# Optimization experiments

Measured on AMD Instinct MI355X. Metric: run time of the kernel, lower is better.

The kernel has to match this reference:

```python
import jax, jax.numpy as jnp
import numpy as np

B, D = 8192, 1024            # batch, inputs_dim
H1, H2, H3 = 2048, 1024, 512 # expert_units
NS, NT = 8, 4                # num_shared_experts, num_tasks_experts
E = NS + 3 * NT              # 20 experts total: [shared 0:8 | SA 8:12 | RA 12:16 | EA 16:20]
TU1, TU2 = 1024, 512         # tower_units
TIN = H3 * 4                 # tower input dim = 2048


def lrelu(x):
    return jnp.where(x >= 0, x, 0.1 * x)


def setup_inputs() -> dict:
    key = jax.random.key(0)
    ks = jax.random.split(key, 24)
    s = 0.02
    return {
        "inputs": jax.random.normal(ks[0], (B, D), jnp.float32),
        # stacked expert MLP params (leading axis = expert index)
        "W1": jax.random.normal(ks[1], (E, D, H1), jnp.float32) * s,
        "b1": jnp.zeros((E, H1), jnp.float32),
        "W2": jax.random.normal(ks[2], (E, H1, H2), jnp.float32) * s,
        "b2": jnp.zeros((E, H2), jnp.float32),
        "W3": jax.random.normal(ks[3], (E, H2, H3), jnp.float32) * s,
        "b3": jnp.zeros((E, H3), jnp.float32),
        # gate linears (single layer + softmax over dim 1)
        "Wg_sh": jax.random.normal(ks[4], (D, NS + 3 * NT), jnp.float32) * s,
        "bg_sh": jnp.zeros((NS + 3 * NT,), jnp.float32),
        "Wg_sa": jax.random.normal(ks[5], (D, NT + NS), jnp.float32) * s,
        "bg_sa": jnp.zeros((NT + NS,), jnp.float32),
        "Wg_ra": jax.random.normal(ks[6], (D, NT + NS), jnp.float32) * s,
        "bg_ra": jnp.zeros((NT + NS,), jnp.float32),
        "Wg_ea": jax.random.normal(ks[7], (D, NT + NS), jnp.float32) * s,
        "bg_ea": jnp.zeros((NT + NS,), jnp.float32),
        # 2 towers (one per task), stacked on leading axis
        "Wt1": jax.random.normal(ks[8], (2, TIN, TU1), jnp.float32) * s,
        "bt1": jnp.zeros((2, TU1), jnp.float32),
        "Wt2": jax.random.normal(ks[9], (2, TU1, TU2), jnp.float32) * s,
        "bt2": jnp.zeros((2, TU2), jnp.float32),
        # per-task output denses: PRESENCE=6, AIRFLOW=4
        "Wd0": jax.random.normal(ks[10], (TU2, 6), jnp.float32) * s,
        "bd0": jnp.zeros((6,), jnp.float32),
        "Wd1": jax.random.normal(ks[11], (TU2, 4), jnp.float32) * s,
        "bd1": jnp.zeros((4,), jnp.float32),
    }


def reference(inputs, W1, b1, W2, b2, W3, b3,
              Wg_sh, bg_sh, Wg_sa, bg_sa, Wg_ra, bg_ra, Wg_ea, bg_ea,
              Wt1, bt1, Wt2, bt2, Wd0, bd0, Wd1, bd1):
    x = inputs
    # all 20 experts as batched GEMMs: [E, B, h]
    h = lrelu(jnp.einsum('bd,edh->ebh', x, W1) + b1[:, None, :])
    h = lrelu(jnp.einsum('ebh,ehk->ebk', h, W2) + b2[:, None, :])
    eo = lrelu(jnp.einsum('ebk,eko->ebo', h, W3) + b3[:, None, :])  # [E,B,H3]

    # gates (softmax over feature dim)
    g_sh = jax.nn.softmax(x @ Wg_sh + bg_sh, axis=1)  # [B, 20]
    g_sa = jax.nn.softmax(x @ Wg_sa + bg_sa, axis=1)  # [B, 12]
    g_ra = jax.nn.softmax(x @ Wg_ra + bg_ra, axis=1)
    g_ea = jax.nn.softmax(x @ Wg_ea + bg_ea, axis=1)

    # shared gate: order = shared + SA + RA + EA == natural stacking order
    out_sh = jnp.einsum('ebh,be->bh', eo, g_sh)
    # task gates: order = task experts + shared experts
    out_sa = jnp.einsum('ebh,be->bh', jnp.concatenate([eo[NS:NS+NT], eo[:NS]], 0), g_sa)
    out_ra = jnp.einsum('ebh,be->bh', jnp.concatenate([eo[NS+NT:NS+2*NT], eo[:NS]], 0), g_ra)
    out_ea = jnp.einsum('ebh,be->bh', jnp.concatenate([eo[NS+2*NT:], eo[:NS]], 0), g_ea)

    tower_in = jnp.concatenate([out_sh, out_sa, out_ra, out_ea], axis=1)  # [B, 2048]
    t = lrelu(jnp.einsum('bi,kio->kbo', tower_in, Wt1) + bt1[:, None, :])  # [2,B,TU1]
    t = lrelu(jnp.einsum('kbo,kop->kbp', t, Wt2) + bt2[:, None, :])        # [2,B,TU2]
    out0 = t[0] @ Wd0 + bd0  # [B, 6]  PRESENCE
    out1 = t[1] @ Wd1 + bd1  # [B, 4]  AIRFLOW
    return (out0, out1)
```

## Files before the change

kernel.cpp:

```cpp
#include <hip/hip_runtime.h>

#define DEV __device__ __forceinline__

typedef __bf16 bf16x8 __attribute__((ext_vector_type(8)));
typedef float f32x4 __attribute__((ext_vector_type(4)));

DEV unsigned short f2bf(float f) {
  union { float f; unsigned u; } v; v.f = f;
  unsigned r = v.u + 0x7FFFu + ((v.u >> 16) & 1u);
  return (unsigned short)(r >> 16);
}
DEV float bf2f(unsigned short h) {
  union { float f; unsigned u; } v; v.u = ((unsigned)h) << 16;
  return v.f;
}

DEV void gload16(const void* g, void* l) {
  __builtin_amdgcn_global_load_lds(
      (__attribute__((address_space(1))) void*)(g),
      (__attribute__((address_space(3))) void*)(l), 16, 0, 0);
}

__global__ __launch_bounds__(512) void gemm256(
    const unsigned short* __restrict__ A,
    const unsigned short* __restrict__ Bt,
    const float* __restrict__ bias,
    unsigned short* __restrict__ Out,
    int N, int K, int nbx, int nby,
    long sA, long sB, long sBias, long sOut)
{
  int wg = blockIdx.x;
  {
    const int nwg = gridDim.x;
    const int q = nwg >> 3, r = nwg & 7;
    const int xcd = wg & 7, pos = wg >> 3;
    wg = (xcd < r ? xcd * (q + 1) : r * (q + 1) + (xcd - r) * q) + pos;
  }
  const int per_z = nbx * nby;
  const int z  = wg / per_z;
  const int rz = wg - z * per_z;
  const int by = rz / nbx;
  const int bx = rz - by * nbx;

  A    += (size_t)z * sA;
  Bt   += (size_t)z * sB;
  bias += (size_t)z * sBias;
  Out  += (size_t)z * sOut;

  const int tid  = threadIdx.x;
  const int lane = tid & 63;
  const int wid  = tid >> 6;
  const int wm   = wid >> 2, wn = wid & 3;
  const int m0   = by * 256, n0 = bx * 256;

  __shared__ alignas(16) char sm[2][65536];

  f32x4 acc[8][4];
  const f32x4 fz = {0.f, 0.f, 0.f, 0.f};
#pragma unroll
  for (int i = 0; i < 8; ++i)
#pragma unroll
    for (int j = 0; j < 4; ++j) acc[i][j] = fz;

  const size_t ldab = (size_t)K * 2;
  const int rr = tid >> 3;
  const int ch = (tid & 7) ^ (rr & 7);
  const char* gA = (const char*)A  + (size_t)(m0 + rr) * ldab + ch * 16;
  const char* gB = (const char*)Bt + (size_t)(n0 + rr) * ldab + ch * 16;
  const size_t rowStep = 64 * ldab;

  const int swz   = (lane & 7) << 4;
  const int kbase = (lane >> 4) << 4;
  const int koff0 = kbase ^ swz;
  const int aRow  = wm * 128 + (lane & 15);
  const int bRow  = wn * 64  + (lane & 15);

  const int nkt = K >> 6;

  auto STAGE = [&](int buf, int kt) {
    const char* sa = gA + (size_t)kt * 128;
    const char* sb = gB + (size_t)kt * 128;
    char* la = sm[buf] + tid * 16;
    char* lb = sm[buf] + 32768 + tid * 16;
#pragma unroll
    for (int j = 0; j < 4; ++j) {
      gload16(sa + j * rowStep, la + j * 8192);
      gload16(sb + j * rowStep, lb + j * 8192);
    }
  };

  STAGE(0, 0);
  int cur = 0;
  for (int kt = 0; kt < nkt; ++kt) {
    if (kt + 1 < nkt) {
      STAGE(cur ^ 1, kt + 1);
      asm volatile("s_waitcnt vmcnt(8)" ::: "memory");
    } else {
      asm volatile("s_waitcnt vmcnt(0)" ::: "memory");
    }
    __builtin_amdgcn_s_barrier();
    __builtin_amdgcn_sched_barrier(0);
    const char* pA = sm[cur] + aRow * 128;
    const char* pB = sm[cur] + 32768 + bRow * 128;
#pragma unroll
    for (int ks = 0; ks < 2; ++ks) {
      const int ko = koff0 ^ (ks * 64);
      bf16x8 af[8], bfr[4];
#pragma unroll
      for (int mi = 0; mi < 8; ++mi) af[mi] = *(const bf16x8*)(pA + mi * 2048 + ko);
#pragma unroll
      for (int ni = 0; ni < 4; ++ni) bfr[ni] = *(const bf16x8*)(pB + ni * 2048 + ko);
#pragma unroll
      for (int mi = 0; mi < 8; ++mi)
#pragma unroll
        for (int ni = 0; ni < 4; ++ni)
          acc[mi][ni] = __builtin_amdgcn_mfma_f32_16x16x32_bf16(
              af[mi], bfr[ni], acc[mi][ni], 0, 0, 0);
    }
    __builtin_amdgcn_sched_barrier(0);
    __builtin_amdgcn_s_barrier();
    cur ^= 1;
  }

#pragma unroll
  for (int ni = 0; ni < 4; ++ni) {
    const int c = n0 + wn * 64 + ni * 16 + (lane & 15);
    const float bv = bias[c];
#pragma unroll
    for (int mi = 0; mi < 8; ++mi) {
      const int r0 = m0 + wm * 128 + mi * 16 + ((lane >> 4) << 2);
#pragma unroll
      for (int j = 0; j < 4; ++j) {
        float v = acc[mi][ni][j] + bv;
        v = v >= 0.f ? v : 0.1f * v;
        Out[(size_t)(r0 + j) * N + c] = f2bf(v);
      }
    }
  }
}

__global__ __launch_bounds__(256) void gemm_bl(
    const unsigned short* __restrict__ A,
    const unsigned short* __restrict__ Bt,
    const float* __restrict__ bias,
    unsigned short* __restrict__ Out,
    int M, int N, int K,
    long sA, long sB, long sBias, long sOut)
{
  A    += (size_t)blockIdx.z * sA;
  Bt   += (size_t)blockIdx.z * sB;
  bias += (size_t)blockIdx.z * sBias;
  Out  += (size_t)blockIdx.z * sOut;

  const int tid  = threadIdx.x;
  const int lane = tid & 63;
  const int wid  = tid >> 6;
  const int wm   = wid >> 1, wn = wid & 1;
  const int m0   = blockIdx.y * 128, n0 = blockIdx.x * 128;

  __shared__ alignas(16) char smA[16384];
  __shared__ alignas(16) char smB[16384];

  f32x4 acc[4][4];
  const f32x4 fz = {0.f, 0.f, 0.f, 0.f};
#pragma unroll
  for (int i = 0; i < 4; ++i)
#pragma unroll
    for (int j = 0; j < 4; ++j) acc[i][j] = fz;

  const size_t ldab = (size_t)K * 2;
  const int rr    = tid >> 3;
  const int chunk = (tid & 7) ^ (rr & 7);
  const char* gA = (const char*)A  + (size_t)(m0 + rr) * ldab + chunk * 16;
  const char* gB = (const char*)Bt + (size_t)(n0 + rr) * ldab + chunk * 16;
  char* lA = smA + tid * 16;
  char* lB = smB + tid * 16;
  const size_t rowStep = 32 * ldab;

  const int swz = (lane & 7) << 4;
  int aoff[4][2], boff[4][2];
#pragma unroll
  for (int f = 0; f < 4; ++f) {
    const int ra = wm * 64 + f * 16 + (lane & 15);
    const int rb = wn * 64 + f * 16 + (lane & 15);
#pragma unroll
    for (int ks = 0; ks < 2; ++ks) {
      const int kb = ks * 64 + ((lane >> 4) << 4);
      aoff[f][ks] = ra * 128 + (kb ^ swz);
      boff[f][ks] = rb * 128 + (kb ^ swz);
    }
  }

  const int nkt = K >> 6;
  for (int kt = 0; kt < nkt; ++kt) {
    const char* sa = gA + (size_t)kt * 128;
    const char* sb = gB + (size_t)kt * 128;
    gload16(sa,               lA);
    gload16(sa +     rowStep, lA + 4096);
    gload16(sa + 2 * rowStep, lA + 8192);
    gload16(sa + 3 * rowStep, lA + 12288);
    gload16(sb,               lB);
    gload16(sb +     rowStep, lB + 4096);
    gload16(sb + 2 * rowStep, lB + 8192);
    gload16(sb + 3 * rowStep, lB + 12288);
    __syncthreads();
#pragma unroll
    for (int ks = 0; ks < 2; ++ks) {
      bf16x8 af[4], bf[4];
#pragma unroll
      for (int f = 0; f < 4; ++f) af[f] = *(const bf16x8*)(smA + aoff[f][ks]);
#pragma unroll
      for (int f = 0; f < 4; ++f) bf[f] = *(const bf16x8*)(smB + boff[f][ks]);
#pragma unroll
      for (int mi = 0; mi < 4; ++mi)
#pragma unroll
        for (int ni = 0; ni < 4; ++ni)
          acc[mi][ni] = __builtin_amdgcn_mfma_f32_16x16x32_bf16(
              af[mi], bf[ni], acc[mi][ni], 0, 0, 0);
    }
    __syncthreads();
  }

#pragma unroll
  for (int ni = 0; ni < 4; ++ni) {
    const int c = n0 + wn * 64 + ni * 16 + (lane & 15);
    const float bv = bias[c];
#pragma unroll
    for (int mi = 0; mi < 4; ++mi) {
#pragma unroll
      for (int j = 0; j < 4; ++j) {
        const int r = m0 + wm * 64 + mi * 16 + ((lane >> 4) << 2) + j;
        float v = acc[mi][ni][j] + bv;
        v = v >= 0.f ? v : 0.1f * v;
        Out[(size_t)r * N + c] = f2bf(v);
      }
    }
  }
}

__global__ __launch_bounds__(256) void conv_t(
    const float* __restrict__ src, unsigned short* __restrict__ dst, int K, int N)
{
  const size_t zo = (size_t)blockIdx.z * K * N;
  src += zo; dst += zo;
  const int k0 = blockIdx.x * 64, n0 = blockIdx.y * 64;
  __shared__ unsigned short lds[64][68];
  const int t = threadIdx.x;
  const int cr = t >> 4;
  const int cc = (t & 15) * 4;
#pragma unroll
  for (int i = 0; i < 4; ++i) {
    const int row = i * 16 + cr;
    const float4 v = *(const float4*)(src + (size_t)(k0 + row) * N + n0 + cc);
    lds[row][cc + 0] = f2bf(v.x); lds[row][cc + 1] = f2bf(v.y);
    lds[row][cc + 2] = f2bf(v.z); lds[row][cc + 3] = f2bf(v.w);
  }
  __syncthreads();
#pragma unroll
  for (int i = 0; i < 4; ++i) {
    const int nrow = i * 16 + cr;
    ushort4 u = make_ushort4(lds[cc + 0][nrow], lds[cc + 1][nrow],
                             lds[cc + 2][nrow], lds[cc + 3][nrow]);
    *(ushort4*)(dst + (size_t)(n0 + nrow) * K + k0 + cc) = u;
  }
}

__global__ __launch_bounds__(256) void conv_x(
    const float* __restrict__ src, unsigned short* __restrict__ dst, int n8)
{
  const int i = blockIdx.x * 256 + threadIdx.x;
  if (i >= n8) return;
  const float4* p = (const float4*)(src + (size_t)i * 8);
  const float4 a = p[0], b = p[1];
  ushort4 u0 = make_ushort4(f2bf(a.x), f2bf(a.y), f2bf(a.z), f2bf(a.w));
  ushort4 u1 = make_ushort4(f2bf(b.x), f2bf(b.y), f2bf(b.z), f2bf(b.w));
  *(ushort4*)(dst + (size_t)i * 8)     = u0;
  *(ushort4*)(dst + (size_t)i * 8 + 4) = u1;
}

__global__ __launch_bounds__(256) void concat_g(
    const float* __restrict__ Wsh, const float* __restrict__ bsh,
    const float* __restrict__ Wsa, const float* __restrict__ bsa,
    const float* __restrict__ Wra, const float* __restrict__ bra,
    const float* __restrict__ Wea, const float* __restrict__ bea,
    float* __restrict__ Wc, float* __restrict__ bc)
{
  const int i = blockIdx.x * 256 + threadIdx.x;
  if (i < 1024 * 56) {
    const int k = i / 56, c = i % 56;
    float v;
    if (c < 20)      v = Wsh[(size_t)k * 20 + c];
    else if (c < 32) v = Wsa[(size_t)k * 12 + (c - 20)];
    else if (c < 44) v = Wra[(size_t)k * 12 + (c - 32)];
    else             v = Wea[(size_t)k * 12 + (c - 44)];
    Wc[i] = v;
  }
  if (i < 64) {
    float v = 0.f;
    if (i < 20)      v = bsh[i];
    else if (i < 32) v = bsa[i - 20];
    else if (i < 44) v = bra[i - 32];
    else if (i < 56) v = bea[i - 44];
    bc[i] = v;
  }
}

__global__ __launch_bounds__(256) void gates_gemm(
    const float* __restrict__ x,
    const float* __restrict__ Wc,
    const float* __restrict__ bc,
    float* __restrict__ logits)
{
  const int b0 = blockIdx.x * 64;
  const int t = threadIdx.x;
  const int tr = t >> 4, tc = t & 15;
  __shared__ float sx[32][64];
  __shared__ float sw[32][64];

  float acc[4][4] = {};

  for (int kt = 0; kt < 32; ++kt) {
    const int k0 = kt * 32;
    __syncthreads();
#pragma unroll
    for (int it = 0; it < 2; ++it) {
      const int idx = t + it * 256;
      const int r = idx >> 3, c4 = (idx & 7) * 4;
      const float4 v = *(const float4*)(x + (size_t)(b0 + r) * 1024 + k0 + c4);
      sx[c4 + 0][r] = v.x; sx[c4 + 1][r] = v.y;
      sx[c4 + 2][r] = v.z; sx[c4 + 3][r] = v.w;
    }
#pragma unroll
    for (int it = 0; it < 2; ++it) {
      const int idx = t + it * 256;
      const int row = idx >> 4;
      const int c4  = (idx & 15) * 4;
      float4 v = {0.f, 0.f, 0.f, 0.f};
      if (c4 < 56)
        v = *(const float4*)(Wc + (size_t)(k0 + row) * 56 + c4);
      *(float4*)&sw[row][c4] = v;
    }
    __syncthreads();
#pragma unroll
    for (int kk = 0; kk < 32; ++kk) {
      const float4 rx = *(const float4*)&sx[kk][tr * 4];
      const float4 wv = *(const float4*)&sw[kk][tc * 4];
#pragma unroll
      for (int i = 0; i < 4; ++i) {
        const float xv = (i == 0) ? rx.x : (i == 1) ? rx.y : (i == 2) ? rx.z : rx.w;
        acc[i][0] += xv * wv.x; acc[i][1] += xv * wv.y;
        acc[i][2] += xv * wv.z; acc[i][3] += xv * wv.w;
      }
    }
  }

  const float4 bv = *(const float4*)&bc[tc * 4];
#pragma unroll
  for (int i = 0; i < 4; ++i) {
    float4 o;
    o.x = acc[i][0] + bv.x; o.y = acc[i][1] + bv.y;
    o.z = acc[i][2] + bv.z; o.w = acc[i][3] + bv.w;
    *(float4*)&logits[(size_t)(b0 + tr * 4 + i) * 64 + tc * 4] = o;
  }
}

__global__ __launch_bounds__(256) void combine_k(
    const unsigned short* __restrict__ eo,
    const float* __restrict__ logits,
    unsigned short* __restrict__ tin)
{
  const int b = blockIdx.x;
  const int t = threadIdx.x;
  __shared__ alignas(16) unsigned short lds[20][512];
  __shared__ float gsm[56];
#pragma unroll
  for (int i = 0; i < 5; ++i) {
    const int chunk = t + i * 256;
    const int e = chunk >> 6;
    const int h0 = (chunk & 63) * 8;
    *(uint4*)&lds[e][h0] = *(const uint4*)(eo + ((size_t)e * 8192 + b) * 512 + h0);
  }
  if (t < 64) {
    const float v0 = (t < 56) ? logits[(size_t)b * 64 + t] : 0.f;
    const int off[4] = {0, 20, 32, 44};
    const int wd[4]  = {20, 12, 12, 12};
    for (int g = 0; g < 4; ++g) {
      const bool in = (t >= off[g]) && (t < off[g] + wd[g]);
      float vv = in ? v0 : -1e30f;
      float m = vv;
#pragma unroll
      for (int o = 32; o; o >>= 1) m = fmaxf(m, __shfl_xor(m, o));
      float e = in ? __expf(vv - m) : 0.f;
      float s = e;
#pragma unroll
      for (int o = 32; o; o >>= 1) s += __shfl_xor(s, o);
      if (in) gsm[t] = e / s;
    }
  }
  __syncthreads();

  const int sec = t >> 6;
  const int h0 = (t & 63) * 8;
  float acc[8] = {0.f, 0.f, 0.f, 0.f, 0.f, 0.f, 0.f, 0.f};
  if (sec == 0) {
    for (int e = 0; e < 20; ++e) {
      const float w = gsm[e];
#pragma unroll
      for (int j = 0; j < 8; ++j) acc[j] += w * bf2f(lds[e][h0 + j]);
    }
  } else {
    const int goff = 20 + (sec - 1) * 12;
    const int ebase = 8 + (sec - 1) * 4;
    for (int tt = 0; tt < 4; ++tt) {
      const float w = gsm[goff + tt];
#pragma unroll
      for (int j = 0; j < 8; ++j) acc[j] += w * bf2f(lds[ebase + tt][h0 + j]);
    }
    for (int ss = 0; ss < 8; ++ss) {
      const float w = gsm[goff + 4 + ss];
#pragma unroll
      for (int j = 0; j < 8; ++j) acc[j] += w * bf2f(lds[ss][h0 + j]);
    }
  }
  unsigned short* ob = tin + (size_t)b * 2048 + sec * 512 + h0;
  ushort4 u0 = make_ushort4(f2bf(acc[0]), f2bf(acc[1]), f2bf(acc[2]), f2bf(acc[3]));
  ushort4 u1 = make_ushort4(f2bf(acc[4]), f2bf(acc[5]), f2bf(acc[6]), f2bf(acc[7]));
  *(ushort4*)ob = u0;
  *(ushort4*)(ob + 4) = u1;
}

__global__ __launch_bounds__(256) void outd_k(
    const unsigned short* __restrict__ t2,
    const float* __restrict__ Wd0, const float* __restrict__ bd0,
    const float* __restrict__ Wd1, const float* __restrict__ bd1,
    float* __restrict__ out)
{
  const int gid = blockIdx.x * 4 + (threadIdx.x >> 6);
  const int lane = threadIdx.x & 63;
  const int b = gid >> 1, task = gid & 1;
  const uint4 raw = *(const uint4*)(t2 + ((size_t)task * 8192 + b) * 512 + lane * 8);
  const unsigned short* rs = (const unsigned short*)&raw;
  float v[8];
#pragma unroll
  for (int j = 0; j < 8; ++j) v[j] = bf2f(rs[j]);
  const float* Wd = task ? Wd1 : Wd0;
  const float* bd = task ? bd1 : bd0;
  const int ncol = task ? 4 : 6;
  float* ob = task ? (out + (size_t)8192 * 6 + (size_t)b * 4) : (out + (size_t)b * 6);
  for (int c = 0; c < ncol; ++c) {
    float p = 0.f;
#pragma unroll
    for (int j = 0; j < 8; ++j) p += v[j] * Wd[(size_t)(lane * 8 + j) * ncol + c];
#pragma unroll
    for (int o = 32; o; o >>= 1) p += __shfl_xor(p, o);
    if (lane == 0) ob[c] = p + bd[c];
  }
}

extern "C" void kernel_launch(void* const* d_in, const int* in_sizes, int n_in,
                              void* d_out, int out_size, void* d_ws, size_t ws_size,
                              hipStream_t stream) {
  const float* x     = (const float*)d_in[0];
  const float* W1    = (const float*)d_in[1];
  const float* b1    = (const float*)d_in[2];
  const float* W2    = (const float*)d_in[3];
  const float* b2    = (const float*)d_in[4];
  const float* W3    = (const float*)d_in[5];
  const float* b3    = (const float*)d_in[6];
  const float* Wg_sh = (const float*)d_in[7];
  const float* bg_sh = (const float*)d_in[8];
  const float* Wg_sa = (const float*)d_in[9];
  const float* bg_sa = (const float*)d_in[10];
  const float* Wg_ra = (const float*)d_in[11];
  const float* bg_ra = (const float*)d_in[12];
  const float* Wg_ea = (const float*)d_in[13];
  const float* bg_ea = (const float*)d_in[14];
  const float* Wt1   = (const float*)d_in[15];
  const float* bt1   = (const float*)d_in[16];
  const float* Wt2   = (const float*)d_in[17];
  const float* bt2   = (const float*)d_in[18];
  const float* Wd0   = (const float*)d_in[19];
  const float* bd0   = (const float*)d_in[20];
  const float* Wd1   = (const float*)d_in[21];
  const float* bd1   = (const float*)d_in[22];
  float* out = (float*)d_out;

  const int B = 8192, D = 1024, H1 = 2048, H2 = 1024, H3 = 512;
  const int E = 20, TU1 = 1024, TU2 = 512, TIN = 2048;

  auto rnd = [](size_t n) { return (n + 255) & ~(size_t)255; };
  const size_t szXb   = rnd((size_t)B * D * 2);
  const size_t szW1t  = rnd((size_t)E * H1 * D * 2);
  const size_t szW2t  = rnd((size_t)E * H2 * H1 * 2);
  const size_t szW3t  = rnd((size_t)E * H3 * H2 * 2);
  const size_t szWt1t = rnd((size_t)2 * TU1 * TIN * 2);
  const size_t szWt2t = rnd((size_t)2 * TU2 * TU1 * 2);
  const size_t szWcat = rnd((size_t)1024 * 56 * 4);
  const size_t szBcat = rnd((size_t)64 * 4);
  const size_t szLog  = rnd((size_t)B * 64 * 4);
  const size_t szEo   = rnd((size_t)E * B * H3 * 2);
  const size_t szTin  = rnd((size_t)B * TIN * 2);
  const size_t szT1   = rnd((size_t)2 * B * TU1 * 2);
  const size_t szT2   = rnd((size_t)2 * B * TU2 * 2);
  const size_t szH1e  = rnd((size_t)B * H1 * 2);
  const size_t szH2e  = rnd((size_t)B * H2 * 2);
  const size_t fixed = szXb + szW1t + szW2t + szW3t + szWt1t + szWt2t +
                       szWcat + szBcat + szLog + szEo;
  const size_t tNeed = szTin + szT1 + szT2;

  int G = 1;
  const int opts[6] = {20, 10, 5, 4, 2, 1};
  for (int i = 0; i < 6; ++i) {
    size_t hNeed = (size_t)opts[i] * (szH1e + szH2e);
    if (hNeed < tNeed) hNeed = tNeed;
    if (fixed + hNeed <= ws_size) { G = opts[i]; break; }
  }

  char* w = (char*)d_ws;
  auto alloc = [&](size_t n) { char* p = w; w += rnd(n); return p; };
  unsigned short* xb   = (unsigned short*)alloc((size_t)B * D * 2);
  unsigned short* W1t  = (unsigned short*)alloc((size_t)E * H1 * D * 2);
  unsigned short* W2t  = (unsigned short*)alloc((size_t)E * H2 * H1 * 2);
  unsigned short* W3t  = (unsigned short*)alloc((size_t)E * H3 * H2 * 2);
  unsigned short* Wt1t = (unsigned short*)alloc((size_t)2 * TU1 * TIN * 2);
  unsigned short* Wt2t = (unsigned short*)alloc((size_t)2 * TU2 * TU1 * 2);
  float*          Wcat = (float*)alloc((size_t)1024 * 56 * 4);
  float*          bcat = (float*)alloc((size_t)64 * 4);
  float*          lgts = (float*)alloc((size_t)B * 64 * 4);
  unsigned short* eo   = (unsigned short*)alloc((size_t)E * B * H3 * 2);
  char* hreg = w;
  unsigned short* h1  = (unsigned short*)hreg;
  unsigned short* h2  = (unsigned short*)(hreg + (size_t)G * szH1e);
  unsigned short* tin = (unsigned short*)hreg;
  unsigned short* t1  = (unsigned short*)(hreg + szTin);
  unsigned short* t2  = (unsigned short*)(hreg + szTin + szT1);
  (void)in_sizes; (void)n_in; (void)out_size;

  auto launch_gemm = [&](const unsigned short* Ap, const unsigned short* Btp,
                         const float* biasp, unsigned short* Outp,
                         int M, int N, int K, int Gz,
                         long sA, long sB, long sBias, long sOut) {
    const int nbx = N / 256, nby = M / 256;
    if (nbx > 0 && (M % 256) == 0 && nbx * nby * Gz >= 200) {
      gemm256<<<dim3(nbx * nby * Gz), 512, 0, stream>>>(
          Ap, Btp, biasp, Outp, N, K, nbx, nby, sA, sB, sBias, sOut);
    } else {
      gemm_bl<<<dim3(N / 128, M / 128, Gz), 256, 0, stream>>>(
          Ap, Btp, biasp, Outp, M, N, K, sA, sB, sBias, sOut);
    }
  };

  conv_x<<<dim3((B * D / 8) / 256), 256, 0, stream>>>(x, xb, B * D / 8);
  conv_t<<<dim3(D / 64,  H1 / 64, E), 256, 0, stream>>>(W1, W1t, D, H1);
  conv_t<<<dim3(H1 / 64, H2 / 64, E), 256, 0, stream>>>(W2, W2t, H1, H2);
  conv_t<<<dim3(H2 / 64, H3 / 64, E), 256, 0, stream>>>(W3, W3t, H2, H3);
  conv_t<<<dim3(TIN / 64, TU1 / 64, 2), 256, 0, stream>>>(Wt1, Wt1t, TIN, TU1);
  conv_t<<<dim3(TU1 / 64, TU2 / 64, 2), 256, 0, stream>>>(Wt2, Wt2t, TU1, TU2);

  concat_g<<<dim3((1024 * 56 + 255) / 256), 256, 0, stream>>>(
      Wg_sh, bg_sh, Wg_sa, bg_sa, Wg_ra, bg_ra, Wg_ea, bg_ea, Wcat, bcat);
  gates_gemm<<<dim3(B / 64), 256, 0, stream>>>(x, Wcat, bcat, lgts);

  for (int e0 = 0; e0 < E; e0 += G) {
    launch_gemm(xb, W1t + (size_t)e0 * H1 * D, b1 + (size_t)e0 * H1, h1,
                B, H1, D, G, 0, (long)H1 * D, (long)H1, (long)B * H1);
    launch_gemm(h1, W2t + (size_t)e0 * H2 * H1, b2 + (size_t)e0 * H2, h2,
                B, H2, H1, G, (long)B * H1, (long)H2 * H1, (long)H2, (long)B * H2);
    launch_gemm(h2, W3t + (size_t)e0 * H3 * H2, b3 + (size_t)e0 * H3,
                eo + (size_t)e0 * B * H3,
                B, H3, H2, G, (long)B * H2, (long)H3 * H2, (long)H3, (long)B * H3);
  }

  combine_k<<<dim3(B), 256, 0, stream>>>(eo, lgts, tin);

  launch_gemm(tin, Wt1t, bt1, t1, B, TU1, TIN, 2,
              0, (long)TU1 * TIN, (long)TU1, (long)B * TU1);
  launch_gemm(t1, Wt2t, bt2, t2, B, TU2, TU1, 2,
              (long)B * TU1, (long)TU2 * TU1, (long)TU2, (long)B * TU2);

  outd_k<<<dim3(B * 2 / 4), 256, 0, stream>>>(t2, Wd0, bd0, Wd1, bd1, out);
}
```

Measured before the change: 2.339 ms.

## Interleave GEMM prefetch with split MFMA phases and store expert outputs batch-major

The 256x256 GEMM main loop is split into four MFMA phases. The global-to-LDS prefetch of the next tile is spread across those phases, with setprio raised around the MFMA blocks so loads overlap with compute. Expert activations are now written interleaved (row stride G*H or E*H3) so the combine kernel reads each batch row contiguously. The small-tile fallback kernel is dropped and every GEMM uses the 256 tile, which adds extra barriers per k-step and risks under-filling the GPU on small launches.

Result: faster. 2.197 ms (-6.1%).

```diff
diff --git a/kernel.cpp b/kernel.cpp
--- a/kernel.cpp
+++ b/kernel.cpp
@@ -20,13 +20,15 @@
       (__attribute__((address_space(1))) void*)(g),
       (__attribute__((address_space(3))) void*)(l), 16, 0, 0);
 }
+
+#define MFMA16(a, b, c) __builtin_amdgcn_mfma_f32_16x16x32_bf16((a), (b), (c), 0, 0, 0)
 
 __global__ __launch_bounds__(512) void gemm256(
     const unsigned short* __restrict__ A,
     const unsigned short* __restrict__ Bt,
     const float* __restrict__ bias,
     unsigned short* __restrict__ Out,
-    int N, int K, int nbx, int nby,
+    int K, int lda, int ldo, int nbx, int nby,
     long sA, long sB, long sBias, long sOut)
 {
   int wg = blockIdx.x;
@@ -62,64 +64,119 @@
 #pragma unroll
     for (int j = 0; j < 4; ++j) acc[i][j] = fz;
 
-  const size_t ldab = (size_t)K * 2;
   const int rr = tid >> 3;
   const int ch = (tid & 7) ^ (rr & 7);
-  const char* gA = (const char*)A  + (size_t)(m0 + rr) * ldab + ch * 16;
-  const char* gB = (const char*)Bt + (size_t)(n0 + rr) * ldab + ch * 16;
-  const size_t rowStep = 64 * ldab;
-
-  const int swz   = (lane & 7) << 4;
-  const int kbase = (lane >> 4) << 4;
-  const int koff0 = kbase ^ swz;
+  const char* gA = (const char*)A  + ((size_t)(m0 + rr) * lda) * 2 + ch * 16;
+  const char* gB = (const char*)Bt + ((size_t)(n0 + rr) * K)   * 2 + ch * 16;
+  const size_t stepA = (size_t)64 * lda * 2;
+  const size_t stepB = (size_t)64 * K * 2;
+
+  const int koff0 = (((lane >> 4) << 4) ^ ((lane & 7) << 4));
   const int aRow  = wm * 128 + (lane & 15);
   const int bRow  = wn * 64  + (lane & 15);
 
   const int nkt = K >> 6;
 
-  auto STAGE = [&](int buf, int kt) {
-    const char* sa = gA + (size_t)kt * 128;
-    const char* sb = gB + (size_t)kt * 128;
-    char* la = sm[buf] + tid * 16;
-    char* lb = sm[buf] + 32768 + tid * 16;
-#pragma unroll
-    for (int j = 0; j < 4; ++j) {
-      gload16(sa + j * rowStep, la + j * 8192);
-      gload16(sb + j * rowStep, lb + j * 8192);
-    }
+  auto SA = [&](int buf, int kt, int jh) {
+    const char* s = gA + (size_t)kt * 128 + (2 * jh) * stepA;
+    char* l = sm[buf] + tid * 16 + (2 * jh) * 8192;
+    gload16(s, l);
+    gload16(s + stepA, l + 8192);
   };
-
-  STAGE(0, 0);
-  int cur = 0;
+  auto SB = [&](int buf, int kt, int jh) {
+    const char* s = gB + (size_t)kt * 128 + (2 * jh) * stepB;
+    char* l = sm[buf] + 32768 + tid * 16 + (2 * jh) * 8192;
+    gload16(s, l);
+    gload16(s + stepB, l + 8192);
+  };
+
+  SA(0, 0, 0); SA(0, 0, 1); SB(0, 0, 0); SB(0, 0, 1);
+
   for (int kt = 0; kt < nkt; ++kt) {
-    if (kt + 1 < nkt) {
-      STAGE(cur ^ 1, kt + 1);
-      asm volatile("s_waitcnt vmcnt(8)" ::: "memory");
+    const int cur = kt & 1, nb = cur ^ 1;
+    const bool pre = (kt + 1 < nkt);
+    if (pre) {
+      SA(nb, kt + 1, 0);
+      asm volatile("s_waitcnt vmcnt(2)" ::: "memory");
     } else {
       asm volatile("s_waitcnt vmcnt(0)" ::: "memory");
     }
     __builtin_amdgcn_s_barrier();
     __builtin_amdgcn_sched_barrier(0);
+
     const char* pA = sm[cur] + aRow * 128;
     const char* pB = sm[cur] + 32768 + bRow * 128;
-#pragma unroll
-    for (int ks = 0; ks < 2; ++ks) {
-      const int ko = koff0 ^ (ks * 64);
-      bf16x8 af[8], bfr[4];
-#pragma unroll
-      for (int mi = 0; mi < 8; ++mi) af[mi] = *(const bf16x8*)(pA + mi * 2048 + ko);
-#pragma unroll
-      for (int ni = 0; ni < 4; ++ni) bfr[ni] = *(const bf16x8*)(pB + ni * 2048 + ko);
-#pragma unroll
-      for (int mi = 0; mi < 8; ++mi)
-#pragma unroll
-        for (int ni = 0; ni < 4; ++ni)
-          acc[mi][ni] = __builtin_amdgcn_mfma_f32_16x16x32_bf16(
-              af[mi], bfr[ni], acc[mi][ni], 0, 0, 0);
-    }
-    __builtin_amdgcn_sched_barrier(0);
-    __builtin_amdgcn_s_barrier();
-    cur ^= 1;
+    bf16x8 a0[4], a1[4], b0[4], b1[4];
+
+    {
+#pragma unroll
+      for (int i = 0; i < 4; ++i) a0[i] = *(const bf16x8*)(pA + i * 2048 + koff0);
+#pragma unroll
+      for (int n = 0; n < 4; ++n) b0[n] = *(const bf16x8*)(pB + n * 2048 + koff0);
+      if (pre) SA(nb, kt + 1, 1);
+      asm volatile("s_waitcnt lgkmcnt(0)" ::: "memory");
+      __builtin_amdgcn_sched_barrier(0);
+      __builtin_amdgcn_s_setprio(1);
+#pragma unroll
+      for (int i = 0; i < 4; ++i)
+#pragma unroll
+        for (int n = 0; n < 4; ++n) acc[i][n] = MFMA16(a0[i], b0[n], acc[i][n]);
+      __builtin_amdgcn_s_setprio(0);
+      __builtin_amdgcn_sched_barrier(0);
+      __builtin_amdgcn_s_barrier();
+      __builtin_amdgcn_sched_barrier(0);
+    }
+    {
+#pragma unroll
+      for (int i = 0; i < 4; ++i) a1[i] = *(const bf16x8*)(pA + (i + 4) * 2048 + koff0);
+      if (pre) SB(nb, kt + 1, 0);
+      asm volatile("s_waitcnt lgkmcnt(0)" ::: "memory");
+      __builtin_amdgcn_sched_barrier(0);
+      __builtin_amdgcn_s_setprio(1);
+#pragma unroll
+      for (int i = 0; i < 4; ++i)
+#pragma unroll
+        for (int n = 0; n < 4; ++n) acc[i + 4][n] = MFMA16(a1[i], b0[n], acc[i + 4][n]);
+      __builtin_amdgcn_s_setprio(0);
+      __builtin_amdgcn_sched_barrier(0);
+      __builtin_amdgcn_s_barrier();
+      __builtin_amdgcn_sched_barrier(0);
+    }
+    {
+      const int ko = koff0 ^ 64;
+#pragma unroll
+      for (int i = 0; i < 4; ++i) a0[i] = *(const bf16x8*)(pA + i * 2048 + ko);
+#pragma unroll
+      for (int n = 0; n < 4; ++n) b1[n] = *(const bf16x8*)(pB + n * 2048 + ko);
+      if (pre) SB(nb, kt + 1, 1);
+      asm volatile("s_waitcnt lgkmcnt(0)" ::: "memory");
+      __builtin_amdgcn_sched_barrier(0);
+      __builtin_amdgcn_s_setprio(1);
+#pragma unroll
+      for (int i = 0; i < 4; ++i)
+#pragma unroll
+        for (int n = 0; n < 4; ++n) acc[i][n] = MFMA16(a0[i], b1[n], acc[i][n]);
+      __builtin_amdgcn_s_setprio(0);
+      __builtin_amdgcn_sched_barrier(0);
+      __builtin_amdgcn_s_barrier();
+      __builtin_amdgcn_sched_barrier(0);
+    }
+    {
+      const int ko = koff0 ^ 64;
+#pragma unroll
+      for (int i = 0; i < 4; ++i) a1[i] = *(const bf16x8*)(pA + (i + 4) * 2048 + ko);
+      asm volatile("s_waitcnt lgkmcnt(0)" ::: "memory");
+      __builtin_amdgcn_sched_barrier(0);
+      __builtin_amdgcn_s_setprio(1);
+#pragma unroll
+      for (int i = 0; i < 4; ++i)
+#pragma unroll
+        for (int n = 0; n < 4; ++n) acc[i + 4][n] = MFMA16(a1[i], b1[n], acc[i + 4][n]);
+      __builtin_amdgcn_s_setprio(0);
+      __builtin_amdgcn_sched_barrier(0);
+      __builtin_amdgcn_s_barrier();
+      __builtin_amdgcn_sched_barrier(0);
+    }
   }
 
 #pragma unroll
@@ -133,106 +190,7 @@
       for (int j = 0; j < 4; ++j) {
         float v = acc[mi][ni][j] + bv;
         v = v >= 0.f ? v : 0.1f * v;
-        Out[(size_t)(r0 + j) * N + c] = f2bf(v);
-      }
-    }
-  }
-}
-
-__global__ __launch_bounds__(256) void gemm_bl(
-    const unsigned short* __restrict__ A,
-    const unsigned short* __restrict__ Bt,
-    const float* __restrict__ bias,
-    unsigned short* __restrict__ Out,
-    int M, int N, int K,
-    long sA, long sB, long sBias, long sOut)
-{
-  A    += (size_t)blockIdx.z * sA;
-  Bt   += (size_t)blockIdx.z * sB;
-  bias += (size_t)blockIdx.z * sBias;
-  Out  += (size_t)blockIdx.z * sOut;
-
-  const int tid  = threadIdx.x;
-  const int lane = tid & 63;
-  const int wid  = tid >> 6;
-  const int wm   = wid >> 1, wn = wid & 1;
-  const int m0   = blockIdx.y * 128, n0 = blockIdx.x * 128;
-
-  __shared__ alignas(16) char smA[16384];
-  __shared__ alignas(16) char smB[16384];
-
-  f32x4 acc[4][4];
-  const f32x4 fz = {0.f, 0.f, 0.f, 0.f};
-#pragma unroll
-  for (int i = 0; i < 4; ++i)
-#pragma unroll
-    for (int j = 0; j < 4; ++j) acc[i][j] = fz;
-
-  const size_t ldab = (size_t)K * 2;
-  const int rr    = tid >> 3;
-  const int chunk = (tid & 7) ^ (rr & 7);
-  const char* gA = (const char*)A  + (size_t)(m0 + rr) * ldab + chunk * 16;
-  const char* gB = (const char*)Bt + (size_t)(n0 + rr) * ldab + chunk * 16;
-  char* lA = smA + tid * 16;
-  char* lB = smB + tid * 16;
-  const size_t rowStep = 32 * ldab;
-
-  const int swz = (lane & 7) << 4;
-  int aoff[4][2], boff[4][2];
-#pragma unroll
-  for (int f = 0; f < 4; ++f) {
-    const int ra = wm * 64 + f * 16 + (lane & 15);
-    const int rb = wn * 64 + f * 16 + (lane & 15);
-#pragma unroll
-    for (int ks = 0; ks < 2; ++ks) {
-      const int kb = ks * 64 + ((lane >> 4) << 4);
-      aoff[f][ks] = ra * 128 + (kb ^ swz);
-      boff[f][ks] = rb * 128 + (kb ^ swz);
-    }
-  }
-
-  const int nkt = K >> 6;
-  for (int kt = 0; kt < nkt; ++kt) {
-    const char* sa = gA + (size_t)kt * 128;
-    const char* sb = gB + (size_t)kt * 128;
-    gload16(sa,               lA);
-    gload16(sa +     rowStep, lA + 4096);
-    gload16(sa + 2 * rowStep, lA + 8192);
-    gload16(sa + 3 * rowStep, lA + 12288);
-    gload16(sb,               lB);
-    gload16(sb +     rowStep, lB + 4096);
-    gload16(sb + 2 * rowStep, lB + 8192);
-    gload16(sb + 3 * rowStep, lB + 12288);
-    __syncthreads();
-#pragma unroll
-    for (int ks = 0; ks < 2; ++ks) {
-      bf16x8 af[4], bf[4];
-#pragma unroll
-      for (int f = 0; f < 4; ++f) af[f] = *(const bf16x8*)(smA + aoff[f][ks]);
-#pragma unroll
-      for (int f = 0; f < 4; ++f) bf[f] = *(const bf16x8*)(smB + boff[f][ks]);
-#pragma unroll
-      for (int mi = 0; mi < 4; ++mi)
-#pragma unroll
-        for (int ni = 0; ni < 4; ++ni)
-          acc[mi][ni] = __builtin_amdgcn_mfma_f32_16x16x32_bf16(
-              af[mi], bf[ni], acc[mi][ni], 0, 0, 0);
-    }
-    __syncthreads();
-  }
-
-#pragma unroll
-  for (int ni = 0; ni < 4; ++ni) {
-    const int c = n0 + wn * 64 + ni * 16 + (lane & 15);
-    const float bv = bias[c];
-#pragma unroll
-    for (int mi = 0; mi < 4; ++mi) {
-#pragma unroll
-      for (int j = 0; j < 4; ++j) {
-        const int r = m0 + wm * 64 + mi * 16 + ((lane >> 4) << 2) + j;
-        float v = acc[mi][ni][j] + bv;
-        v = v >= 0.f ? v : 0.1f * v;
-        Out[(size_t)r * N + c] = f2bf(v);
+        Out[(size_t)(r0 + j) * ldo + c] = f2bf(v);
       }
     }
   }
@@ -373,12 +331,12 @@
   const int t = threadIdx.x;
   __shared__ alignas(16) unsigned short lds[20][512];
   __shared__ float gsm[56];
+  const unsigned short* er = eo + (size_t)b * 10240;
+  unsigned short* ldsf = &lds[0][0];
 #pragma unroll
   for (int i = 0; i < 5; ++i) {
-    const int chunk = t + i * 256;
-    const int e = chunk >> 6;
-    const int h0 = (chunk & 63) * 8;
-    *(uint4*)&lds[e][h0] = *(const uint4*)(eo + ((size_t)e * 8192 + b) * 512 + h0);
+    const int c = t + i * 256;
+    *(uint4*)&ldsf[c * 8] = *(const uint4*)(er + c * 8);
   }
   if (t < 64) {
     const float v0 = (t < 56) ? logits[(size_t)b * 64 + t] : 0.f;
@@ -536,18 +494,14 @@
   unsigned short* t2  = (unsigned short*)(hreg + szTin + szT1);
   (void)in_sizes; (void)n_in; (void)out_size;
 
-  auto launch_gemm = [&](const unsigned short* Ap, const unsigned short* Btp,
-                         const float* biasp, unsigned short* Outp,
-                         int M, int N, int K, int Gz,
-                         long sA, long sB, long sBias, long sOut) {
-    const int nbx = N / 256, nby = M / 256;
-    if (nbx > 0 && (M % 256) == 0 && nbx * nby * Gz >= 200) {
-      gemm256<<<dim3(nbx * nby * Gz), 512, 0, stream>>>(
-          Ap, Btp, biasp, Outp, N, K, nbx, nby, sA, sB, sBias, sOut);
-    } else {
-      gemm_bl<<<dim3(N / 128, M / 128, Gz), 256, 0, stream>>>(
-          Ap, Btp, biasp, Outp, M, N, K, sA, sB, sBias, sOut);
-    }
+  auto launch256 = [&](const unsigned short* Ap, int lda, long sA,
+                       const unsigned short* Btp, long sB,
+                       const float* biasp, long sBias,
+                       unsigned short* Outp, int ldo, long sOut,
+                       int N, int K, int nz) {
+    const int nbx = N / 256, nby = B / 256;
+    gemm256<<<dim3(nbx * nby * nz), 512, 0, stream>>>(
+        Ap, Btp, biasp, Outp, K, lda, ldo, nbx, nby, sA, sB, sBias, sOut);
   };
 
   conv_x<<<dim3((B * D / 8) / 256), 256, 0, stream>>>(x, xb, B * D / 8);
@@ -562,21 +516,26 @@
   gates_gemm<<<dim3(B / 64), 256, 0, stream>>>(x, Wcat, bcat, lgts);
 
   for (int e0 = 0; e0 < E; e0 += G) {
-    launch_gemm(xb, W1t + (size_t)e0 * H1 * D, b1 + (size_t)e0 * H1, h1,
-                B, H1, D, G, 0, (long)H1 * D, (long)H1, (long)B * H1);
-    launch_gemm(h1, W2t + (size_t)e0 * H2 * H1, b2 + (size_t)e0 * H2, h2,
-                B, H2, H1, G, (long)B * H1, (long)H2 * H1, (long)H2, (long)B * H2);
-    launch_gemm(h2, W3t + (size_t)e0 * H3 * H2, b3 + (size_t)e0 * H3,
-                eo + (size_t)e0 * B * H3,
-                B, H3, H2, G, (long)B * H2, (long)H3 * H2, (long)H3, (long)B * H3);
+    launch256(xb, D, 0,
+              W1t + (size_t)e0 * H1 * D, (long)H1 * D,
+              b1 + (size_t)e0 * H1, H1,
+              h1, G * H1, H1, H1, D, G);
+    launch256(h1, G * H1, H1,
+              W2t + (size_t)e0 * H2 * H1, (long)H2 * H1,
+              b2 + (size_t)e0 * H2, H2,
+              h2, G * H2, H2, H2, H1, G);
+    launch256(h2, G * H2, H2,
+              W3t + (size_t)e0 * H3 * H2, (long)H3 * H2,
+              b3 + (size_t)e0 * H3, H3,
+              eo + (size_t)e0 * H3, E * H3, H3, H3, H2, G);
   }
 
   combine_k<<<dim3(B), 256, 0, stream>>>(eo, lgts, tin);
 
-  launch_gemm(tin, Wt1t, bt1, t1, B, TU1, TIN, 2,
-              0, (long)TU1 * TIN, (long)TU1, (long)B * TU1);
-  launch_gemm(t1, Wt2t, bt2, t2, B, TU2, TU1, 2,
-              (long)B * TU1, (long)TU2 * TU1, (long)TU2, (long)B * TU2);
+  launch256(tin, TIN, 0, Wt1t, (long)TU1 * TIN, bt1, TU1,
+            t1, TU1, (long)B * TU1, TU1, TIN, 2);
+  launch256(t1, TU1, (long)B * TU1, Wt2t, (long)TU2 * TU1, bt2, TU2,
+            t2, TU2, (long)B * TU2, TU2, TU1, 2);
 
   outd_k<<<dim3(B * 2 / 4), 256, 0, stream>>>(t2, Wd0, bd0, Wd1, bd1, out);
 }
```
